# Kernel tuning notes

Hardware: AMD Instinct MI355X
Metric: run time of the kernel (lower is better)

Reference implementation:

```python
import math
import jax, jax.numpy as jnp
import numpy as np

B, T, D, H = 8, 1024, 256, 8
DH = D // H


def setup_inputs() -> dict:
    key = jax.random.key(0)
    ks = jax.random.split(key, 12)
    s = 0.05
    return {
        "query": jax.random.normal(ks[0], (B, T, D), jnp.float32),
        "Wq": jax.random.normal(ks[1], (D, D), jnp.float32) * s,
        "bq": jnp.zeros((D,), jnp.float32),
        "Wk": jax.random.normal(ks[2], (D, D), jnp.float32) * s,
        "bk": jnp.zeros((D,), jnp.float32),
        "Wv": jax.random.normal(ks[3], (D, D), jnp.float32) * s,
        "bv": jnp.zeros((D,), jnp.float32),
        "Wp": jax.random.normal(ks[4], (D, D), jnp.float32) * s,
        "Wo": jax.random.normal(ks[5], (D, D), jnp.float32) * s,
        "bo": jnp.zeros((D,), jnp.float32),
        "u_bias": jax.random.normal(ks[6], (H, DH), jnp.float32) * s,
        "v_bias": jax.random.normal(ks[7], (H, DH), jnp.float32) * s,
    }


def _rel_pos_encoding(T, D, dtype):
    # sinusoidal PE for relative positions -T+1 .. T-1  -> [2T-1, D]
    positions = jnp.arange(-T + 1, T, dtype=dtype)[:, None]          # [2T-1, 1]
    denom = jnp.exp(jnp.arange(0, D, 2, dtype=dtype) * (-math.log(10000.0) / D))
    ang = positions * denom                                           # [2T-1, D/2]
    # even dims = sin, odd dims = cos (interleaved)
    return jnp.stack([jnp.sin(ang), jnp.cos(ang)], axis=-1).reshape(2 * T - 1, D)


def reference(query, Wq, bq, Wk, bk, Wv, bv, Wp, Wo, bo, u_bias, v_bias):
    B_, T_, D_ = query.shape
    H_ = u_bias.shape[0]
    dh = D_ // H_
    scale = math.sqrt(D_)

    pe = _rel_pos_encoding(T_, D_, query.dtype)                       # [2T-1, D]
    P = (pe @ Wp.T).reshape(2 * T_ - 1, H_, dh)                       # [2T-1, H, dh]

    q = (query @ Wq.T + bq).reshape(B_, T_, H_, dh)                   # [B,T,H,dh]
    k = (query @ Wk.T + bk).reshape(B_, T_, H_, dh)
    v = (query @ Wv.T + bv).reshape(B_, T_, H_, dh)

    content = jnp.einsum('bihd,bjhd->bhij', q + u_bias, k)            # [B,H,T,T]

    # pos_score[b,h,i,j] = sum_d (q+v_bias)[b,i,h,d] * P[i-j+T-1,h,d]
    M = jnp.einsum('bihd,rhd->bhir', q + v_bias, P)                   # [B,H,T,2T-1]
    idx = (jnp.arange(T_)[:, None] - jnp.arange(T_)[None, :]) + (T_ - 1)  # [T,T]
    pos = jnp.take_along_axis(M, idx[None, None], axis=-1)            # [B,H,T,T]

    attn = jax.nn.softmax((content + pos) / scale, axis=-1)           # [B,H,T,T]
    out = jnp.einsum('bhij,bjhd->bihd', attn, v).reshape(B_, T_, D_)
    return out @ Wo.T + bo, attn
```

## Files before the change

kernel.cpp:

```cpp
#include <hip/hip_runtime.h>
#include <math.h>

#define TSEQ   1024
#define DMODEL 256
#define NHEAD  8
#define DHEAD  32
#define NREL   2047
#define OUT0   2097152

#define Q_OFF   0u
#define K_OFF   2097152u
#define V_OFF   4194304u
#define P_OFF   6291456u
#define O_OFF   6815488u
#define PE_OFF  8912640u

__global__ __launch_bounds__(256) void pe_kernel(float* __restrict__ pe) {
  int idx = blockIdx.x * 256 + threadIdx.x;
  int r = idx >> 8;
  int col = idx & 255;
  int m2 = col >> 1;
  float denom = exp2f((float)m2 * -0.10381025296523007f);
  float ang = (float)(r - 1023) * denom;
  pe[idx] = (col & 1) ? cosf(ang) : sinf(ang);
}

__global__ __launch_bounds__(256) void proj_qkv_kernel(
    const float* __restrict__ X,
    const float* __restrict__ Wq, const float* __restrict__ Wk, const float* __restrict__ Wv,
    const float* __restrict__ bq, const float* __restrict__ bk, const float* __restrict__ bv,
    float* __restrict__ qbuf, float* __restrict__ kbuf, float* __restrict__ vbuf)
{
  __shared__ float Xs[32][68];
  __shared__ float Ws[32][68];
  const int bm = blockIdx.x;
  const int bn = blockIdx.y;
  const int sel = bn >> 2;
  const float* W   = sel == 0 ? Wq : (sel == 1 ? Wk : Wv);
  const float* bia = sel == 0 ? bq : (sel == 1 ? bk : bv);
  float* dst       = sel == 0 ? qbuf : (sel == 1 ? kbuf : vbuf);
  const int c0  = (bn & 3) * 64;
  const int bt0 = bm * 64;
  const int tid = threadIdx.x;
  const int tx = tid & 15, ty = tid >> 4;
  float acc[4][4] = {};

  for (int k0 = 0; k0 < 256; k0 += 32) {
    __syncthreads();
    int c = tid;
    for (int l = 0; l < 2; ++l, c += 256) {
      int row = c >> 3, kq = (c & 7) * 4;
      float4 x4 = *(const float4*)&X[(size_t)(bt0 + row) * 256 + k0 + kq];
      Xs[kq + 0][row] = x4.x; Xs[kq + 1][row] = x4.y;
      Xs[kq + 2][row] = x4.z; Xs[kq + 3][row] = x4.w;
    }
    c = tid;
    for (int l = 0; l < 2; ++l, c += 256) {
      int row = c >> 3, kq = (c & 7) * 4;
      float4 w4 = *(const float4*)&W[(size_t)(c0 + row) * 256 + k0 + kq];
      Ws[kq + 0][row] = w4.x; Ws[kq + 1][row] = w4.y;
      Ws[kq + 2][row] = w4.z; Ws[kq + 3][row] = w4.w;
    }
    __syncthreads();
#pragma unroll
    for (int kk = 0; kk < 32; ++kk) {
      float4 a4 = *(const float4*)&Xs[kk][ty * 4];
      float4 b4 = *(const float4*)&Ws[kk][tx * 4];
      float av[4] = {a4.x, a4.y, a4.z, a4.w};
      float bv_[4] = {b4.x, b4.y, b4.z, b4.w};
#pragma unroll
      for (int i = 0; i < 4; ++i)
#pragma unroll
        for (int j = 0; j < 4; ++j) acc[i][j] += av[i] * bv_[j];
    }
  }
#pragma unroll
  for (int j = 0; j < 4; ++j) {
    int dcol = c0 + tx * 4 + j;
    float bz = bia[dcol];
    int hh = dcol >> 5, dd = dcol & 31;
#pragma unroll
    for (int i = 0; i < 4; ++i) {
      int bt = bt0 + ty * 4 + i;
      int bb = bt >> 10, t = bt & 1023;
      dst[(((size_t)bb * NHEAD + hh) * TSEQ + t) * DHEAD + dd] = acc[i][j] + bz;
    }
  }
}

__global__ __launch_bounds__(256) void pgemm_kernel(
    const float* __restrict__ pe, const float* __restrict__ Wp, float* __restrict__ pbuf)
{
  __shared__ float Xs[32][68];
  __shared__ float Ws[32][68];
  const int bm = blockIdx.x;
  const int bn = blockIdx.y;
  const int c0  = bn * 64;
  const int bt0 = bm * 64;
  const int tid = threadIdx.x;
  const int tx = tid & 15, ty = tid >> 4;
  float acc[4][4] = {};

  for (int k0 = 0; k0 < 256; k0 += 32) {
    __syncthreads();
    int c = tid;
    for (int l = 0; l < 2; ++l, c += 256) {
      int row = c >> 3, kq = (c & 7) * 4;
      int rgg = bt0 + row; if (rgg > 2046) rgg = 2046;
      float4 x4 = *(const float4*)&pe[(size_t)rgg * 256 + k0 + kq];
      Xs[kq + 0][row] = x4.x; Xs[kq + 1][row] = x4.y;
      Xs[kq + 2][row] = x4.z; Xs[kq + 3][row] = x4.w;
    }
    c = tid;
    for (int l = 0; l < 2; ++l, c += 256) {
      int row = c >> 3, kq = (c & 7) * 4;
      float4 w4 = *(const float4*)&Wp[(size_t)(c0 + row) * 256 + k0 + kq];
      Ws[kq + 0][row] = w4.x; Ws[kq + 1][row] = w4.y;
      Ws[kq + 2][row] = w4.z; Ws[kq + 3][row] = w4.w;
    }
    __syncthreads();
#pragma unroll
    for (int kk = 0; kk < 32; ++kk) {
      float4 a4 = *(const float4*)&Xs[kk][ty * 4];
      float4 b4 = *(const float4*)&Ws[kk][tx * 4];
      float av[4] = {a4.x, a4.y, a4.z, a4.w};
      float bv_[4] = {b4.x, b4.y, b4.z, b4.w};
#pragma unroll
      for (int i = 0; i < 4; ++i)
#pragma unroll
        for (int j = 0; j < 4; ++j) acc[i][j] += av[i] * bv_[j];
    }
  }
#pragma unroll
  for (int j = 0; j < 4; ++j) {
    int dcol = c0 + tx * 4 + j;
    int hh = dcol >> 5, dd = dcol & 31;
#pragma unroll
    for (int i = 0; i < 4; ++i) {
      int rr = bt0 + ty * 4 + i;
      if (rr < NREL) pbuf[((size_t)hh * NREL + rr) * DHEAD + dd] = acc[i][j];
    }
  }
}

__global__ __launch_bounds__(256, 2) void attn_kernel(
    const float* __restrict__ qbuf, const float* __restrict__ kbuf, const float* __restrict__ vbuf,
    const float* __restrict__ pbuf, const float* __restrict__ ub, const float* __restrict__ vbias,
    float* __restrict__ attn_out, float* __restrict__ obuf)
{
  __shared__ float smem[15744];
  float* const quT = smem;
  float* const qvT = smem + 640;
  float* const BT  = smem + 1280;
  float* const MR  = smem + 9600;

  const int blk = blockIdx.x;
  const int bh  = blk >> 6;
  const int i0  = (blk & 63) << 4;
  const int h   = bh & 7;
  const int bb  = bh >> 3;
  const int tid = threadIdx.x;

  const float* __restrict__ qrow = qbuf + (size_t)bh * (TSEQ * DHEAD);
  const float* __restrict__ krow = kbuf + (size_t)bh * (TSEQ * DHEAD);
  const float* __restrict__ vrow = vbuf + (size_t)bh * (TSEQ * DHEAD);
  const float* __restrict__ Ph   = pbuf + (size_t)h * ((size_t)NREL * DHEAD);
  float* __restrict__ arow = attn_out + (size_t)bh * ((size_t)TSEQ * TSEQ);

  if (tid < 128) {
    const int ri = tid >> 3, dq = (tid & 7) * 4;
    const float4 q4 = *(const float4*)&qrow[(size_t)(i0 + ri) * DHEAD + dq];
    const float4 u4 = *(const float4*)&ub[h * DHEAD + dq];
    const float4 w4 = *(const float4*)&vbias[h * DHEAD + dq];
    quT[(dq + 0) * 20 + ri] = q4.x + u4.x;
    quT[(dq + 1) * 20 + ri] = q4.y + u4.y;
    quT[(dq + 2) * 20 + ri] = q4.z + u4.z;
    quT[(dq + 3) * 20 + ri] = q4.w + u4.w;
    qvT[(dq + 0) * 20 + ri] = q4.x + w4.x;
    qvT[(dq + 1) * 20 + ri] = q4.y + w4.y;
    qvT[(dq + 2) * 20 + ri] = q4.z + w4.z;
    qvT[(dq + 3) * 20 + ri] = q4.w + w4.w;
  }

  const int rg   = tid >> 6;
  const int cg   = tid & 63;
  const bool isM = (cg >= 32);
  const int bcol = cg * 4;
  const float* const Aptr = (isM ? qvT : quT) + rg * 4;

  const int lr    = tid >> 1;
  const int lhalf = (tid & 1) * 16;

  float s[64];

  {
#pragma unroll
    for (int seg = 0; seg < 2; ++seg) {
      const int g = i0 + seg * 128 + lr;
      const float* src = &Ph[(size_t)g * DHEAD + lhalf];
      const int col = seg * 128 + lr;
#pragma unroll
      for (int l = 0; l < 4; ++l) {
        const float4 x = *(const float4*)&src[l * 4];
        const int dq = lhalf + l * 4;
        BT[(dq + 0) * 260 + col] = x.x;
        BT[(dq + 1) * 260 + col] = x.y;
        BT[(dq + 2) * 260 + col] = x.z;
        BT[(dq + 3) * 260 + col] = x.w;
      }
    }
    __syncthreads();
    float acc[4][4] = {};
    const float* Apre = qvT + rg * 4;
#pragma unroll 8
    for (int kk = 0; kk < 32; ++kk) {
      const float4 a4 = *(const float4*)&Apre[kk * 20];
      const float4 b4 = *(const float4*)&BT[kk * 260 + bcol];
      const float av[4] = {a4.x, a4.y, a4.z, a4.w};
      const float bw[4] = {b4.x, b4.y, b4.z, b4.w};
#pragma unroll
      for (int rr = 0; rr < 4; ++rr)
#pragma unroll
        for (int jj = 0; jj < 4; ++jj) acc[rr][jj] += av[rr] * bw[jj];
    }
    float* const Md = MR + (cg >> 5) * 2048 + (cg & 31) * 4;
#pragma unroll
    for (int rr = 0; rr < 4; ++rr)
      *(float4*)&Md[(rg * 4 + rr) * 128] =
          make_float4(acc[rr][0], acc[rr][1], acc[rr][2], acc[rr][3]);
    __syncthreads();
  }

#pragma unroll
  for (int t = 7; t >= 0; --t) {
    const int j0 = t * 128;
    const int cnext = 9 - t;
    {
      const float* srck = &krow[(size_t)(j0 + lr) * DHEAD + lhalf];
      int g = i0 + cnext * 128 + lr;
      if (g > 2046) g = 2046;
      const float* srcp = &Ph[(size_t)g * DHEAD + lhalf];
#pragma unroll
      for (int l = 0; l < 4; ++l) {
        const float4 xk = *(const float4*)&srck[l * 4];
        const float4 xp = *(const float4*)&srcp[l * 4];
        const int dq = lhalf + l * 4;
        BT[(dq + 0) * 260 + lr] = xk.x;
        BT[(dq + 1) * 260 + lr] = xk.y;
        BT[(dq + 2) * 260 + lr] = xk.z;
        BT[(dq + 3) * 260 + lr] = xk.w;
        BT[(dq + 0) * 260 + 128 + lr] = xp.x;
        BT[(dq + 1) * 260 + 128 + lr] = xp.y;
        BT[(dq + 2) * 260 + 128 + lr] = xp.z;
        BT[(dq + 3) * 260 + 128 + lr] = xp.w;
      }
    }
    __syncthreads();
    float acc[4][4] = {};
#pragma unroll 8
    for (int kk = 0; kk < 32; ++kk) {
      const float4 a4 = *(const float4*)&Aptr[kk * 20];
      const float4 b4 = *(const float4*)&BT[kk * 260 + bcol];
      const float av[4] = {a4.x, a4.y, a4.z, a4.w};
      const float bw[4] = {b4.x, b4.y, b4.z, b4.w};
#pragma unroll
      for (int rr = 0; rr < 4; ++rr)
#pragma unroll
        for (int jj = 0; jj < 4; ++jj) acc[rr][jj] += av[rr] * bw[jj];
    }
    if (isM) {
      float* const Md = MR + (cnext % 3) * 2048 + (cg & 31) * 4;
#pragma unroll
      for (int rr = 0; rr < 4; ++rr)
        *(float4*)&Md[(rg * 4 + rr) * 128] =
            make_float4(acc[rr][0], acc[rr][1], acc[rr][2], acc[rr][3]);
    } else {
      const float* const Mlo = MR + ((7 - t) % 3) * 2048;
      const float* const Mhi = MR + ((8 - t) % 3) * 2048;
      const int thr  = (8 - t) * 128;
      const int rbas = rg * 4 - bcol + 1023 - j0;
#pragma unroll
      for (int rr = 0; rr < 4; ++rr) {
        const int i = rg * 4 + rr;
#pragma unroll
        for (int jj = 0; jj < 4; ++jj) {
          const int rl = rbas + rr - jj;
          const float* Mp = (rl >= thr) ? Mhi : Mlo;
          acc[rr][jj] += Mp[i * 128 + (rl & 127)];
        }
      }
    }
    __syncthreads();
    float* const Sx = MR + ((7 - t) % 3) * 2048;
    if (!isM) {
#pragma unroll
      for (int rr = 0; rr < 4; ++rr) {
        const int i = rg * 4 + rr;
        const int colb = (bcol + 4 * i) & 127;
        *(float4*)&Sx[i * 128 + colb] =
            make_float4(acc[rr][0], acc[rr][1], acc[rr][2], acc[rr][3]);
      }
    }
    __syncthreads();
    {
      const int rr2 = tid >> 4, u2 = tid & 15;
#pragma unroll
      for (int k2 = 0; k2 < 2; ++k2) {
        const int colb = ((u2 * 8 + k2 * 4) + 4 * rr2) & 127;
        const float4 v4 = *(const float4*)&Sx[rr2 * 128 + colb];
        s[t * 8 + k2 * 4 + 0] = v4.x;
        s[t * 8 + k2 * 4 + 1] = v4.y;
        s[t * 8 + k2 * 4 + 2] = v4.z;
        s[t * 8 + k2 * 4 + 3] = v4.w;
      }
    }
  }

  const int r  = tid >> 4;
  const int u2 = tid & 15;
  float mx = -1e30f;
#pragma unroll
  for (int k = 0; k < 64; ++k) mx = fmaxf(mx, s[k]);
  mx = fmaxf(mx, __shfl_xor(mx, 1));
  mx = fmaxf(mx, __shfl_xor(mx, 2));
  mx = fmaxf(mx, __shfl_xor(mx, 4));
  mx = fmaxf(mx, __shfl_xor(mx, 8));
  const float ksc = 0.09016844136f;
  float sum = 0.f;
#pragma unroll
  for (int k = 0; k < 64; ++k) {
    const float p = exp2f((s[k] - mx) * ksc);
    s[k] = p;
    sum += p;
  }
  sum += __shfl_xor(sum, 1);
  sum += __shfl_xor(sum, 2);
  sum += __shfl_xor(sum, 4);
  sum += __shfl_xor(sum, 8);
  const float rcpl = 1.0f / sum;

  float* const Vs = BT;
  float* const Px = MR;
  const int rq   = tid >> 6;
  const int dsec = (tid >> 4) & 3;
  const int uu   = tid & 15;
  float oa[4][8] = {};

#pragma unroll
  for (int t2 = 0; t2 < 8; ++t2) {
    const int j0 = t2 * 128;
    __syncthreads();
#pragma unroll
    for (int l = 0; l < 4; ++l) {
      const int idx = tid + 256 * l;
      const int row = idx >> 3, dq = (idx & 7) * 4;
      const float4 v4 = *(const float4*)&vrow[(size_t)(j0 + row) * DHEAD + dq];
      *(float2*)&Vs[row * 34 + dq]     = make_float2(v4.x, v4.y);
      *(float2*)&Vs[row * 34 + dq + 2] = make_float2(v4.z, v4.w);
    }
    {
      float pv[8];
#pragma unroll
      for (int k = 0; k < 8; ++k) pv[k] = s[t2 * 8 + k] * rcpl;
      float* gp = &arow[(size_t)(i0 + r) * TSEQ + j0 + u2 * 8];
      *(float4*)&gp[0] = make_float4(pv[0], pv[1], pv[2], pv[3]);
      *(float4*)&gp[4] = make_float4(pv[4], pv[5], pv[6], pv[7]);
      const int c0b = ((u2 * 8)     + 4 * r) & 127;
      const int c1b = ((u2 * 8 + 4) + 4 * r) & 127;
      *(float4*)&Px[r * 128 + c0b] = make_float4(pv[0], pv[1], pv[2], pv[3]);
      *(float4*)&Px[r * 128 + c1b] = make_float4(pv[4], pv[5], pv[6], pv[7]);
    }
    __syncthreads();
#pragma unroll
    for (int jj = 0; jj < 8; ++jj) {
      const int j = uu + 16 * jj;
      float pr[4];
#pragma unroll
      for (int rr = 0; rr < 4; ++rr) {
        const int i = rq * 4 + rr;
        pr[rr] = Px[i * 128 + ((j + 4 * i) & 127)];
      }
      float vv[8];
#pragma unroll
      for (int k2 = 0; k2 < 4; ++k2)
        *(float2*)&vv[k2 * 2] = *(const float2*)&Vs[j * 34 + dsec * 8 + k2 * 2];
#pragma unroll
      for (int rr = 0; rr < 4; ++rr)
#pragma unroll
        for (int dd = 0; dd < 8; ++dd)
          oa[rr][dd] += pr[rr] * vv[dd];
    }
  }

  __syncthreads();
  float* const part = BT;
#pragma unroll
  for (int rr = 0; rr < 4; ++rr) {
    const int i = rq * 4 + rr;
    float* dst = &part[uu * 516 + i * 32 + dsec * 8];
    *(float4*)&dst[0] = make_float4(oa[rr][0], oa[rr][1], oa[rr][2], oa[rr][3]);
    *(float4*)&dst[4] = make_float4(oa[rr][4], oa[rr][5], oa[rr][6], oa[rr][7]);
  }
  __syncthreads();
#pragma unroll
  for (int w2 = 0; w2 < 2; ++w2) {
    const int o = tid + 256 * w2;
    float v = 0.f;
#pragma unroll
    for (int u3 = 0; u3 < 16; ++u3) v += part[u3 * 516 + o];
    const int orow = o >> 5, od = o & 31;
    obuf[((size_t)bb * TSEQ + i0 + orow) * DMODEL + h * DHEAD + od] = v;
  }
}

__global__ __launch_bounds__(256) void oproj_kernel(
    const float* __restrict__ A, const float* __restrict__ Wo, const float* __restrict__ bo,
    float* __restrict__ out)
{
  __shared__ float Xs[32][68];
  __shared__ float Ws[32][68];
  const int bm = blockIdx.x;
  const int bn = blockIdx.y;
  const int c0  = bn * 64;
  const int bt0 = bm * 64;
  const int tid = threadIdx.x;
  const int tx = tid & 15, ty = tid >> 4;
  float acc[4][4] = {};

  for (int k0 = 0; k0 < 256; k0 += 32) {
    __syncthreads();
    int c = tid;
    for (int l = 0; l < 2; ++l, c += 256) {
      int row = c >> 3, kq = (c & 7) * 4;
      float4 x4 = *(const float4*)&A[(size_t)(bt0 + row) * 256 + k0 + kq];
      Xs[kq + 0][row] = x4.x; Xs[kq + 1][row] = x4.y;
      Xs[kq + 2][row] = x4.z; Xs[kq + 3][row] = x4.w;
    }
    c = tid;
    for (int l = 0; l < 2; ++l, c += 256) {
      int row = c >> 3, kq = (c & 7) * 4;
      float4 w4 = *(const float4*)&Wo[(size_t)(c0 + row) * 256 + k0 + kq];
      Ws[kq + 0][row] = w4.x; Ws[kq + 1][row] = w4.y;
      Ws[kq + 2][row] = w4.z; Ws[kq + 3][row] = w4.w;
    }
    __syncthreads();
#pragma unroll
    for (int kk = 0; kk < 32; ++kk) {
      float4 a4 = *(const float4*)&Xs[kk][ty * 4];
      float4 b4 = *(const float4*)&Ws[kk][tx * 4];
      float av[4] = {a4.x, a4.y, a4.z, a4.w};
      float bv_[4] = {b4.x, b4.y, b4.z, b4.w};
#pragma unroll
      for (int i = 0; i < 4; ++i)
#pragma unroll
        for (int j = 0; j < 4; ++j) acc[i][j] += av[i] * bv_[j];
    }
  }
#pragma unroll
  for (int j = 0; j < 4; ++j) {
    int dcol = c0 + tx * 4 + j;
    float bz = bo[dcol];
#pragma unroll
    for (int i = 0; i < 4; ++i) {
      int bt = bt0 + ty * 4 + i;
      out[(size_t)bt * DMODEL + dcol] = acc[i][j] + bz;
    }
  }
}

extern "C" void kernel_launch(void* const* d_in, const int* in_sizes, int n_in,
                              void* d_out, int out_size, void* d_ws, size_t ws_size,
                              hipStream_t stream) {
  const float* X   = (const float*)d_in[0];
  const float* Wq  = (const float*)d_in[1];
  const float* bq  = (const float*)d_in[2];
  const float* Wk  = (const float*)d_in[3];
  const float* bk  = (const float*)d_in[4];
  const float* Wv  = (const float*)d_in[5];
  const float* bv  = (const float*)d_in[6];
  const float* Wp  = (const float*)d_in[7];
  const float* Wo  = (const float*)d_in[8];
  const float* bo  = (const float*)d_in[9];
  const float* ub  = (const float*)d_in[10];
  const float* vbb = (const float*)d_in[11];

  float* ws = (float*)d_ws;
  float* qbuf = ws + Q_OFF;
  float* kbuf = ws + K_OFF;
  float* vbuf = ws + V_OFF;
  float* pbuf = ws + P_OFF;
  float* obuf = ws + O_OFF;
  float* pe   = ws + PE_OFF;

  float* out0 = (float*)d_out;
  float* attn = out0 + OUT0;

  pe_kernel<<<2047, 256, 0, stream>>>(pe);
  proj_qkv_kernel<<<dim3(128, 12), 256, 0, stream>>>(X, Wq, Wk, Wv, bq, bk, bv,
                                                     qbuf, kbuf, vbuf);
  pgemm_kernel<<<dim3(32, 4), 256, 0, stream>>>(pe, Wp, pbuf);
  attn_kernel<<<4096, 256, 0, stream>>>(qbuf, kbuf, vbuf, pbuf, ub, vbb, attn, obuf);
  oproj_kernel<<<dim3(128, 4), 256, 0, stream>>>(obuf, Wo, bo, out0);
}
```

Before: 652.1 us.

## Rewrite attention with split-bf16 MFMA and two-pass online softmax

```diff
diff --git a/kernel.cpp b/kernel.cpp
--- a/kernel.cpp
+++ b/kernel.cpp
@@ -14,6 +14,30 @@
 #define P_OFF   6291456u
 #define O_OFF   6815488u
 #define PE_OFF  8912640u
+
+typedef __attribute__((ext_vector_type(8))) short bf16x8;
+typedef __attribute__((ext_vector_type(4))) float f32x4;
+
+#define MFMA16 __builtin_amdgcn_mfma_f32_16x16x32_bf16
+
+__device__ __forceinline__ void split2(float x, unsigned short& h, unsigned short& l) {
+  unsigned u = __float_as_uint(x);
+  unsigned r = (u + 0x7fffu + ((u >> 16) & 1u)) >> 16;
+  h = (unsigned short)r;
+  float res = x - __uint_as_float(r << 16);
+  unsigned u2 = __float_as_uint(res);
+  l = (unsigned short)((u2 + 0x7fffu + ((u2 >> 16) & 1u)) >> 16);
+}
+
+__device__ __forceinline__ void cvt8(const float* x, bf16x8& h8, bf16x8& l8) {
+#pragma unroll
+  for (int e = 0; e < 8; ++e) {
+    unsigned short a, b;
+    split2(x[e], a, b);
+    h8[e] = (short)a;
+    l8[e] = (short)b;
+  }
+}
 
 __global__ __launch_bounds__(256) void pe_kernel(float* __restrict__ pe) {
   int idx = blockIdx.x * 256 + threadIdx.x;
@@ -29,7 +53,8 @@
     const float* __restrict__ X,
     const float* __restrict__ Wq, const float* __restrict__ Wk, const float* __restrict__ Wv,
     const float* __restrict__ bq, const float* __restrict__ bk, const float* __restrict__ bv,
-    float* __restrict__ qbuf, float* __restrict__ kbuf, float* __restrict__ vbuf)
+    float* __restrict__ qbuf, unsigned short* __restrict__ khi,
+    unsigned short* __restrict__ klo, float* __restrict__ vbuf)
 {
   __shared__ float Xs[32][68];
   __shared__ float Ws[32][68];
@@ -38,7 +63,7 @@
   const int sel = bn >> 2;
   const float* W   = sel == 0 ? Wq : (sel == 1 ? Wk : Wv);
   const float* bia = sel == 0 ? bq : (sel == 1 ? bk : bv);
-  float* dst       = sel == 0 ? qbuf : (sel == 1 ? kbuf : vbuf);
+  float* fdst      = sel == 0 ? qbuf : vbuf;
   const int c0  = (bn & 3) * 64;
   const int bt0 = bm * 64;
   const int tid = threadIdx.x;
@@ -83,13 +108,23 @@
     for (int i = 0; i < 4; ++i) {
       int bt = bt0 + ty * 4 + i;
       int bb = bt >> 10, t = bt & 1023;
-      dst[(((size_t)bb * NHEAD + hh) * TSEQ + t) * DHEAD + dd] = acc[i][j] + bz;
+      const size_t o = (((size_t)bb * NHEAD + hh) * TSEQ + t) * DHEAD + dd;
+      const float val = acc[i][j] + bz;
+      if (sel == 1) {
+        unsigned short a2, b2;
+        split2(val, a2, b2);
+        khi[o] = a2;
+        klo[o] = b2;
+      } else {
+        fdst[o] = val;
+      }
     }
   }
 }
 
 __global__ __launch_bounds__(256) void pgemm_kernel(
-    const float* __restrict__ pe, const float* __restrict__ Wp, float* __restrict__ pbuf)
+    const float* __restrict__ pe, const float* __restrict__ Wp,
+    unsigned short* __restrict__ phi, unsigned short* __restrict__ plo)
 {
   __shared__ float Xs[32][68];
   __shared__ float Ws[32][68];
@@ -138,278 +173,253 @@
 #pragma unroll
     for (int i = 0; i < 4; ++i) {
       int rr = bt0 + ty * 4 + i;
-      if (rr < NREL) pbuf[((size_t)hh * NREL + rr) * DHEAD + dd] = acc[i][j];
+      if (rr < NREL) {
+        unsigned short a2, b2;
+        split2(acc[i][j], a2, b2);
+        const size_t o = ((size_t)hh * NREL + rr) * DHEAD + dd;
+        phi[o] = a2;
+        plo[o] = b2;
+      }
     }
   }
 }
 
 __global__ __launch_bounds__(256, 2) void attn_kernel(
-    const float* __restrict__ qbuf, const float* __restrict__ kbuf, const float* __restrict__ vbuf,
-    const float* __restrict__ pbuf, const float* __restrict__ ub, const float* __restrict__ vbias,
+    const float* __restrict__ qbuf,
+    const unsigned short* __restrict__ khi, const unsigned short* __restrict__ klo,
+    const float* __restrict__ vbuf,
+    const unsigned short* __restrict__ phi, const unsigned short* __restrict__ plo,
+    const float* __restrict__ ub, const float* __restrict__ vbias,
     float* __restrict__ attn_out, float* __restrict__ obuf)
 {
-  __shared__ float smem[15744];
-  float* const quT = smem;
-  float* const qvT = smem + 640;
-  float* const BT  = smem + 1280;
-  float* const MR  = smem + 9600;
-
-  const int blk = blockIdx.x;
-  const int bh  = blk >> 6;
-  const int i0  = (blk & 63) << 4;
-  const int h   = bh & 7;
-  const int bb  = bh >> 3;
-  const int tid = threadIdx.x;
+  __shared__ float smem[14976];
+  float* const Mlds = smem;
+  float* const Pt   = smem + 8448;
+  float* const VT   = smem + 12800;
+
+  const int orig = blockIdx.x;
+  const int blk  = (orig & 7) * 128 + (orig >> 3);
+  const int bh   = blk >> 4;
+  const int i0   = (blk & 15) << 6;
+  const int h    = bh & 7;
+  const int bb   = bh >> 3;
+  const int tid  = threadIdx.x;
+  const int w    = tid >> 6;
+  const int lane = tid & 63;
+  const int lc   = lane & 15;
+  const int lg   = lane >> 4;
 
   const float* __restrict__ qrow = qbuf + (size_t)bh * (TSEQ * DHEAD);
-  const float* __restrict__ krow = kbuf + (size_t)bh * (TSEQ * DHEAD);
+  const unsigned short* __restrict__ kh = khi + (size_t)bh * (TSEQ * DHEAD);
+  const unsigned short* __restrict__ kl = klo + (size_t)bh * (TSEQ * DHEAD);
   const float* __restrict__ vrow = vbuf + (size_t)bh * (TSEQ * DHEAD);
-  const float* __restrict__ Ph   = pbuf + (size_t)h * ((size_t)NREL * DHEAD);
+  const unsigned short* __restrict__ ph_ = phi + (size_t)h * ((size_t)NREL * DHEAD);
+  const unsigned short* __restrict__ pl_ = plo + (size_t)h * ((size_t)NREL * DHEAD);
   float* __restrict__ arow = attn_out + (size_t)bh * ((size_t)TSEQ * TSEQ);
 
-  if (tid < 128) {
-    const int ri = tid >> 3, dq = (tid & 7) * 4;
-    const float4 q4 = *(const float4*)&qrow[(size_t)(i0 + ri) * DHEAD + dq];
-    const float4 u4 = *(const float4*)&ub[h * DHEAD + dq];
-    const float4 w4 = *(const float4*)&vbias[h * DHEAD + dq];
-    quT[(dq + 0) * 20 + ri] = q4.x + u4.x;
-    quT[(dq + 1) * 20 + ri] = q4.y + u4.y;
-    quT[(dq + 2) * 20 + ri] = q4.z + u4.z;
-    quT[(dq + 3) * 20 + ri] = q4.w + u4.w;
-    qvT[(dq + 0) * 20 + ri] = q4.x + w4.x;
-    qvT[(dq + 1) * 20 + ri] = q4.y + w4.y;
-    qvT[(dq + 2) * 20 + ri] = q4.z + w4.z;
-    qvT[(dq + 3) * 20 + ri] = q4.w + w4.w;
-  }
-
-  const int rg   = tid >> 6;
-  const int cg   = tid & 63;
-  const bool isM = (cg >= 32);
-  const int bcol = cg * 4;
-  const float* const Aptr = (isM ? qvT : quT) + rg * 4;
-
-  const int lr    = tid >> 1;
-  const int lhalf = (tid & 1) * 16;
-
-  float s[64];
-
+  bf16x8 quh, qul, qvh, qvl;
   {
-#pragma unroll
-    for (int seg = 0; seg < 2; ++seg) {
-      const int g = i0 + seg * 128 + lr;
-      const float* src = &Ph[(size_t)g * DHEAD + lhalf];
-      const int col = seg * 128 + lr;
-#pragma unroll
-      for (int l = 0; l < 4; ++l) {
-        const float4 x = *(const float4*)&src[l * 4];
-        const int dq = lhalf + l * 4;
-        BT[(dq + 0) * 260 + col] = x.x;
-        BT[(dq + 1) * 260 + col] = x.y;
-        BT[(dq + 2) * 260 + col] = x.z;
-        BT[(dq + 3) * 260 + col] = x.w;
+    float q8[8];
+    const float* qp = &qrow[(size_t)(i0 + 16 * w + lc) * DHEAD + 8 * lg];
+    *(float4*)&q8[0] = *(const float4*)&qp[0];
+    *(float4*)&q8[4] = *(const float4*)&qp[4];
+#pragma unroll
+    for (int e = 0; e < 8; ++e) {
+      const float uu = ub[h * DHEAD + 8 * lg + e];
+      const float vv = vbias[h * DHEAD + 8 * lg + e];
+      unsigned short a, b;
+      split2(q8[e] + uu, a, b); quh[e] = (short)a; qul[e] = (short)b;
+      split2(q8[e] + vv, a, b); qvh[e] = (short)a; qvl[e] = (short)b;
+    }
+  }
+
+  const float KSC = 0.09016844136f;
+  float m_l[4], sm_l[4];
+#pragma unroll
+  for (int r = 0; r < 4; ++r) { m_l[r] = -1e30f; sm_l[r] = 0.f; }
+
+  const f32x4 zf = {0.f, 0.f, 0.f, 0.f};
+
+  for (int t = 0; t < 16; ++t) {
+    const int j0 = t * 64;
+    const int r0 = i0 - j0 + 960;
+    f32x4 mf[8];
+#pragma unroll
+    for (int st = 0; st < 8; ++st) mf[st] = zf;
+#pragma unroll
+    for (int st = 0; st < 8; ++st) {
+      int pr = r0 + 16 * st + lc;
+      if (pr > 2046) pr = 2046;
+      const size_t o = (size_t)pr * DHEAD + 8 * lg;
+      const bf16x8 bh8 = *(const bf16x8*)&ph_[o];
+      const bf16x8 bl8 = *(const bf16x8*)&pl_[o];
+      mf[st] = MFMA16(qvh, bh8, mf[st], 0, 0, 0);
+      mf[st] = MFMA16(qvl, bh8, mf[st], 0, 0, 0);
+      mf[st] = MFMA16(qvh, bl8, mf[st], 0, 0, 0);
+    }
+    __syncthreads();
+#pragma unroll
+    for (int st = 0; st < 8; ++st)
+#pragma unroll
+      for (int r = 0; r < 4; ++r)
+        Mlds[(16 * w + 4 * lg + r) * 132 + 16 * st + lc] = mf[st][r];
+
+    f32x4 sf[4];
+#pragma unroll
+    for (int st = 0; st < 4; ++st) sf[st] = zf;
+#pragma unroll
+    for (int st = 0; st < 4; ++st) {
+      const size_t o = (size_t)(j0 + 16 * st + lc) * DHEAD + 8 * lg;
+      const bf16x8 bh8 = *(const bf16x8*)&kh[o];
+      const bf16x8 bl8 = *(const bf16x8*)&kl[o];
+      sf[st] = MFMA16(quh, bh8, sf[st], 0, 0, 0);
+      sf[st] = MFMA16(qul, bh8, sf[st], 0, 0, 0);
+      sf[st] = MFMA16(quh, bl8, sf[st], 0, 0, 0);
+    }
+    __syncthreads();
+#pragma unroll
+    for (int st = 0; st < 4; ++st) {
+      const int jloc = 16 * st + lc;
+#pragma unroll
+      for (int r = 0; r < 4; ++r) {
+        const int il = 16 * w + 4 * lg + r;
+        sf[st][r] += Mlds[il * 132 + (il - jloc + 63)];
       }
     }
-    __syncthreads();
-    float acc[4][4] = {};
-    const float* Apre = qvT + rg * 4;
-#pragma unroll 8
-    for (int kk = 0; kk < 32; ++kk) {
-      const float4 a4 = *(const float4*)&Apre[kk * 20];
-      const float4 b4 = *(const float4*)&BT[kk * 260 + bcol];
-      const float av[4] = {a4.x, a4.y, a4.z, a4.w};
-      const float bw[4] = {b4.x, b4.y, b4.z, b4.w};
-#pragma unroll
-      for (int rr = 0; rr < 4; ++rr)
-#pragma unroll
-        for (int jj = 0; jj < 4; ++jj) acc[rr][jj] += av[rr] * bw[jj];
-    }
-    float* const Md = MR + (cg >> 5) * 2048 + (cg & 31) * 4;
-#pragma unroll
-    for (int rr = 0; rr < 4; ++rr)
-      *(float4*)&Md[(rg * 4 + rr) * 128] =
-          make_float4(acc[rr][0], acc[rr][1], acc[rr][2], acc[rr][3]);
-    __syncthreads();
-  }
-
-#pragma unroll
-  for (int t = 7; t >= 0; --t) {
-    const int j0 = t * 128;
-    const int cnext = 9 - t;
+#pragma unroll
+    for (int r = 0; r < 4; ++r) {
+      const float t0 = fmaxf(fmaxf(sf[0][r], sf[1][r]), fmaxf(sf[2][r], sf[3][r]));
+      const float mn = fmaxf(m_l[r], t0);
+      const float ps = exp2f((sf[0][r] - mn) * KSC) + exp2f((sf[1][r] - mn) * KSC)
+                     + exp2f((sf[2][r] - mn) * KSC) + exp2f((sf[3][r] - mn) * KSC);
+      sm_l[r] = sm_l[r] * exp2f((m_l[r] - mn) * KSC) + ps;
+      m_l[r] = mn;
+    }
+  }
+
+  float m_f[4], rs[4];
+#pragma unroll
+  for (int r = 0; r < 4; ++r) {
+    float mm = m_l[r], ss = sm_l[r];
+#pragma unroll
+    for (int d = 1; d < 16; d <<= 1) {
+      const float om = __shfl_xor(mm, d);
+      const float os = __shfl_xor(ss, d);
+      const float M2 = fmaxf(mm, om);
+      ss = ss * exp2f((mm - M2) * KSC) + os * exp2f((om - M2) * KSC);
+      mm = M2;
+    }
+    m_f[r] = mm;
+    rs[r] = 1.0f / ss;
+  }
+
+  f32x4 of0 = zf, of1 = zf;
+  for (int t = 0; t < 16; ++t) {
+    const int j0 = t * 64;
+    const int r0 = i0 - j0 + 960;
+    const int idxv = tid * 2;
+    const int vr1 = idxv >> 3, vd1 = (idxv & 7) * 4;
+    const int vr2 = (idxv + 1) >> 3, vd2 = ((idxv + 1) & 7) * 4;
+    const float4 va  = *(const float4*)&vrow[(size_t)(j0 + vr1) * DHEAD + vd1];
+    const float4 vb4 = *(const float4*)&vrow[(size_t)(j0 + vr2) * DHEAD + vd2];
+
+    f32x4 mf[8];
+#pragma unroll
+    for (int st = 0; st < 8; ++st) mf[st] = zf;
+#pragma unroll
+    for (int st = 0; st < 8; ++st) {
+      int pr = r0 + 16 * st + lc;
+      if (pr > 2046) pr = 2046;
+      const size_t o = (size_t)pr * DHEAD + 8 * lg;
+      const bf16x8 bh8 = *(const bf16x8*)&ph_[o];
+      const bf16x8 bl8 = *(const bf16x8*)&pl_[o];
+      mf[st] = MFMA16(qvh, bh8, mf[st], 0, 0, 0);
+      mf[st] = MFMA16(qvl, bh8, mf[st], 0, 0, 0);
+      mf[st] = MFMA16(qvh, bl8, mf[st], 0, 0, 0);
+    }
+    __syncthreads();
+#pragma unroll
+    for (int st = 0; st < 8; ++st)
+#pragma unroll
+      for (int r = 0; r < 4; ++r)
+        Mlds[(16 * w + 4 * lg + r) * 132 + 16 * st + lc] = mf[st][r];
+    VT[(vd1 + 0) * 68 + vr1] = va.x;
+    VT[(vd1 + 1) * 68 + vr1] = va.y;
+    VT[(vd1 + 2) * 68 + vr1] = va.z;
+    VT[(vd1 + 3) * 68 + vr1] = va.w;
+    VT[(vd2 + 0) * 68 + vr2] = vb4.x;
+    VT[(vd2 + 1) * 68 + vr2] = vb4.y;
+    VT[(vd2 + 2) * 68 + vr2] = vb4.z;
+    VT[(vd2 + 3) * 68 + vr2] = vb4.w;
+
+    f32x4 sf[4];
+#pragma unroll
+    for (int st = 0; st < 4; ++st) sf[st] = zf;
+#pragma unroll
+    for (int st = 0; st < 4; ++st) {
+      const size_t o = (size_t)(j0 + 16 * st + lc) * DHEAD + 8 * lg;
+      const bf16x8 bh8 = *(const bf16x8*)&kh[o];
+      const bf16x8 bl8 = *(const bf16x8*)&kl[o];
+      sf[st] = MFMA16(quh, bh8, sf[st], 0, 0, 0);
+      sf[st] = MFMA16(qul, bh8, sf[st], 0, 0, 0);
+      sf[st] = MFMA16(quh, bl8, sf[st], 0, 0, 0);
+    }
+    __syncthreads();
+#pragma unroll
+    for (int st = 0; st < 4; ++st) {
+      const int jloc = 16 * st + lc;
+#pragma unroll
+      for (int r = 0; r < 4; ++r) {
+        const int il = 16 * w + 4 * lg + r;
+        const float sv = sf[st][r] + Mlds[il * 132 + (il - jloc + 63)];
+        const float p = exp2f((sv - m_f[r]) * KSC) * rs[r];
+        Pt[il * 68 + jloc] = p;
+      }
+    }
+    __syncthreads();
     {
-      const float* srck = &krow[(size_t)(j0 + lr) * DHEAD + lhalf];
-      int g = i0 + cnext * 128 + lr;
-      if (g > 2046) g = 2046;
-      const float* srcp = &Ph[(size_t)g * DHEAD + lhalf];
-#pragma unroll
-      for (int l = 0; l < 4; ++l) {
-        const float4 xk = *(const float4*)&srck[l * 4];
-        const float4 xp = *(const float4*)&srcp[l * 4];
-        const int dq = lhalf + l * 4;
-        BT[(dq + 0) * 260 + lr] = xk.x;
-        BT[(dq + 1) * 260 + lr] = xk.y;
-        BT[(dq + 2) * 260 + lr] = xk.z;
-        BT[(dq + 3) * 260 + lr] = xk.w;
-        BT[(dq + 0) * 260 + 128 + lr] = xp.x;
-        BT[(dq + 1) * 260 + 128 + lr] = xp.y;
-        BT[(dq + 2) * 260 + 128 + lr] = xp.z;
-        BT[(dq + 3) * 260 + 128 + lr] = xp.w;
-      }
-    }
-    __syncthreads();
-    float acc[4][4] = {};
-#pragma unroll 8
-    for (int kk = 0; kk < 32; ++kk) {
-      const float4 a4 = *(const float4*)&Aptr[kk * 20];
-      const float4 b4 = *(const float4*)&BT[kk * 260 + bcol];
-      const float av[4] = {a4.x, a4.y, a4.z, a4.w};
-      const float bw[4] = {b4.x, b4.y, b4.z, b4.w};
-#pragma unroll
-      for (int rr = 0; rr < 4; ++rr)
-#pragma unroll
-        for (int jj = 0; jj < 4; ++jj) acc[rr][jj] += av[rr] * bw[jj];
-    }
-    if (isM) {
-      float* const Md = MR + (cnext % 3) * 2048 + (cg & 31) * 4;
-#pragma unroll
-      for (int rr = 0; rr < 4; ++rr)
-        *(float4*)&Md[(rg * 4 + rr) * 128] =
-            make_float4(acc[rr][0], acc[rr][1], acc[rr][2], acc[rr][3]);
-    } else {
-      const float* const Mlo = MR + ((7 - t) % 3) * 2048;
-      const float* const Mhi = MR + ((8 - t) % 3) * 2048;
-      const int thr  = (8 - t) * 128;
-      const int rbas = rg * 4 - bcol + 1023 - j0;
-#pragma unroll
-      for (int rr = 0; rr < 4; ++rr) {
-        const int i = rg * 4 + rr;
-#pragma unroll
-        for (int jj = 0; jj < 4; ++jj) {
-          const int rl = rbas + rr - jj;
-          const float* Mp = (rl >= thr) ? Mhi : Mlo;
-          acc[rr][jj] += Mp[i * 128 + (rl & 127)];
+      const int prow = tid >> 2, cb = (tid & 3) * 16;
+      float* gp = &arow[(size_t)(i0 + prow) * TSEQ + j0 + cb];
+      const float* sp = &Pt[prow * 68 + cb];
+#pragma unroll
+      for (int qq = 0; qq < 4; ++qq)
+        *(float4*)&gp[qq * 4] = *(const float4*)&sp[qq * 4];
+    }
+#pragma unroll
+    for (int kc = 0; kc < 2; ++kc) {
+      float tmp[8];
+      const float* ap = &Pt[(16 * w + lc) * 68 + 32 * kc + 8 * lg];
+      *(float4*)&tmp[0] = *(const float4*)&ap[0];
+      *(float4*)&tmp[4] = *(const float4*)&ap[4];
+      bf16x8 ah, al;
+      cvt8(tmp, ah, al);
+#pragma unroll
+      for (int ds = 0; ds < 2; ++ds) {
+        float tv[8];
+        const float* vp = &VT[(lc + 16 * ds) * 68 + 32 * kc + 8 * lg];
+        *(float4*)&tv[0] = *(const float4*)&vp[0];
+        *(float4*)&tv[4] = *(const float4*)&vp[4];
+        bf16x8 vh, vl;
+        cvt8(tv, vh, vl);
+        if (ds == 0) {
+          of0 = MFMA16(ah, vh, of0, 0, 0, 0);
+          of0 = MFMA16(al, vh, of0, 0, 0, 0);
+          of0 = MFMA16(ah, vl, of0, 0, 0, 0);
+        } else {
+          of1 = MFMA16(ah, vh, of1, 0, 0, 0);
+          of1 = MFMA16(al, vh, of1, 0, 0, 0);
+          of1 = MFMA16(ah, vl, of1, 0, 0, 0);
         }
       }
     }
-    __syncthreads();
-    float* const Sx = MR + ((7 - t) % 3) * 2048;
-    if (!isM) {
-#pragma unroll
-      for (int rr = 0; rr < 4; ++rr) {
-        const int i = rg * 4 + rr;
-        const int colb = (bcol + 4 * i) & 127;
-        *(float4*)&Sx[i * 128 + colb] =
-            make_float4(acc[rr][0], acc[rr][1], acc[rr][2], acc[rr][3]);
-      }
-    }
-    __syncthreads();
-    {
-      const int rr2 = tid >> 4, u2 = tid & 15;
-#pragma unroll
-      for (int k2 = 0; k2 < 2; ++k2) {
-        const int colb = ((u2 * 8 + k2 * 4) + 4 * rr2) & 127;
-        const float4 v4 = *(const float4*)&Sx[rr2 * 128 + colb];
-        s[t * 8 + k2 * 4 + 0] = v4.x;
-        s[t * 8 + k2 * 4 + 1] = v4.y;
-        s[t * 8 + k2 * 4 + 2] = v4.z;
-        s[t * 8 + k2 * 4 + 3] = v4.w;
-      }
-    }
-  }
-
-  const int r  = tid >> 4;
-  const int u2 = tid & 15;
-  float mx = -1e30f;
-#pragma unroll
-  for (int k = 0; k < 64; ++k) mx = fmaxf(mx, s[k]);
-  mx = fmaxf(mx, __shfl_xor(mx, 1));
-  mx = fmaxf(mx, __shfl_xor(mx, 2));
-  mx = fmaxf(mx, __shfl_xor(mx, 4));
-  mx = fmaxf(mx, __shfl_xor(mx, 8));
-  const float ksc = 0.09016844136f;
-  float sum = 0.f;
-#pragma unroll
-  for (int k = 0; k < 64; ++k) {
-    const float p = exp2f((s[k] - mx) * ksc);
-    s[k] = p;
-    sum += p;
-  }
-  sum += __shfl_xor(sum, 1);
-  sum += __shfl_xor(sum, 2);
-  sum += __shfl_xor(sum, 4);
-  sum += __shfl_xor(sum, 8);
-  const float rcpl = 1.0f / sum;
-
-  float* const Vs = BT;
-  float* const Px = MR;
-  const int rq   = tid >> 6;
-  const int dsec = (tid >> 4) & 3;
-  const int uu   = tid & 15;
-  float oa[4][8] = {};
-
-#pragma unroll
-  for (int t2 = 0; t2 < 8; ++t2) {
-    const int j0 = t2 * 128;
-    __syncthreads();
-#pragma unroll
-    for (int l = 0; l < 4; ++l) {
-      const int idx = tid + 256 * l;
-      const int row = idx >> 3, dq = (idx & 7) * 4;
-      const float4 v4 = *(const float4*)&vrow[(size_t)(j0 + row) * DHEAD + dq];
-      *(float2*)&Vs[row * 34 + dq]     = make_float2(v4.x, v4.y);
-      *(float2*)&Vs[row * 34 + dq + 2] = make_float2(v4.z, v4.w);
-    }
-    {
-      float pv[8];
-#pragma unroll
-      for (int k = 0; k < 8; ++k) pv[k] = s[t2 * 8 + k] * rcpl;
-      float* gp = &arow[(size_t)(i0 + r) * TSEQ + j0 + u2 * 8];
-      *(float4*)&gp[0] = make_float4(pv[0], pv[1], pv[2], pv[3]);
-      *(float4*)&gp[4] = make_float4(pv[4], pv[5], pv[6], pv[7]);
-      const int c0b = ((u2 * 8)     + 4 * r) & 127;
-      const int c1b = ((u2 * 8 + 4) + 4 * r) & 127;
-      *(float4*)&Px[r * 128 + c0b] = make_float4(pv[0], pv[1], pv[2], pv[3]);
-      *(float4*)&Px[r * 128 + c1b] = make_float4(pv[4], pv[5], pv[6], pv[7]);
-    }
-    __syncthreads();
-#pragma unroll
-    for (int jj = 0; jj < 8; ++jj) {
-      const int j = uu + 16 * jj;
-      float pr[4];
-#pragma unroll
-      for (int rr = 0; rr < 4; ++rr) {
-        const int i = rq * 4 + rr;
-        pr[rr] = Px[i * 128 + ((j + 4 * i) & 127)];
-      }
-      float vv[8];
-#pragma unroll
-      for (int k2 = 0; k2 < 4; ++k2)
-        *(float2*)&vv[k2 * 2] = *(const float2*)&Vs[j * 34 + dsec * 8 + k2 * 2];
-#pragma unroll
-      for (int rr = 0; rr < 4; ++rr)
-#pragma unroll
-        for (int dd = 0; dd < 8; ++dd)
-          oa[rr][dd] += pr[rr] * vv[dd];
-    }
-  }
-
-  __syncthreads();
-  float* const part = BT;
-#pragma unroll
-  for (int rr = 0; rr < 4; ++rr) {
-    const int i = rq * 4 + rr;
-    float* dst = &part[uu * 516 + i * 32 + dsec * 8];
-    *(float4*)&dst[0] = make_float4(oa[rr][0], oa[rr][1], oa[rr][2], oa[rr][3]);
-    *(float4*)&dst[4] = make_float4(oa[rr][4], oa[rr][5], oa[rr][6], oa[rr][7]);
-  }
-  __syncthreads();
-#pragma unroll
-  for (int w2 = 0; w2 < 2; ++w2) {
-    const int o = tid + 256 * w2;
-    float v = 0.f;
-#pragma unroll
-    for (int u3 = 0; u3 < 16; ++u3) v += part[u3 * 516 + o];
-    const int orow = o >> 5, od = o & 31;
-    obuf[((size_t)bb * TSEQ + i0 + orow) * DMODEL + h * DHEAD + od] = v;
+  }
+
+#pragma unroll
+  for (int r = 0; r < 4; ++r) {
+    const int row = i0 + 16 * w + 4 * lg + r;
+    float* op = &obuf[((size_t)bb * TSEQ + row) * DMODEL + h * DHEAD];
+    op[lc]      = of0[r];
+    op[lc + 16] = of1[r];
   }
 }
 
@@ -486,9 +496,11 @@
 
   float* ws = (float*)d_ws;
   float* qbuf = ws + Q_OFF;
-  float* kbuf = ws + K_OFF;
+  unsigned short* khi = (unsigned short*)(ws + K_OFF);
+  unsigned short* klo = khi + 2097152u;
   float* vbuf = ws + V_OFF;
-  float* pbuf = ws + P_OFF;
+  unsigned short* phi = (unsigned short*)(ws + P_OFF);
+  unsigned short* plo = phi + 524032u;
   float* obuf = ws + O_OFF;
   float* pe   = ws + PE_OFF;
 
@@ -497,8 +509,9 @@
 
   pe_kernel<<<2047, 256, 0, stream>>>(pe);
   proj_qkv_kernel<<<dim3(128, 12), 256, 0, stream>>>(X, Wq, Wk, Wv, bq, bk, bv,
-                                                     qbuf, kbuf, vbuf);
-  pgemm_kernel<<<dim3(32, 4), 256, 0, stream>>>(pe, Wp, pbuf);
-  attn_kernel<<<4096, 256, 0, stream>>>(qbuf, kbuf, vbuf, pbuf, ub, vbb, attn, obuf);
+                                                     qbuf, khi, klo, vbuf);
+  pgemm_kernel<<<dim3(32, 4), 256, 0, stream>>>(pe, Wp, phi, plo);
+  attn_kernel<<<1024, 256, 0, stream>>>(qbuf, khi, klo, vbuf, phi, plo, ub, vbb,
+                                        attn, obuf);
   oproj_kernel<<<dim3(128, 4), 256, 0, stream>>>(obuf, Wo, bo, out0);
 }
```

Result: faster. 577.2 us (-11.5%).
